# Kernel optimization log

Hardware: AMD Instinct MI355X
Metric: run time of the kernel (lower is better)

The kernel has to match this reference:

```python
import jax, jax.numpy as jnp
import numpy as np

# dims
B, T, E = 2, 4096, 512
H = 8
DH = E // H            # 64 per-head dim
DEPTH = 4
NHASH = 4              # n_hashes
BUCKET = 64            # bucket_size
NB = T // BUCKET       # n_buckets = 64 (even)
VOCAB, NCLASS = 32000, 10
FF = 4 * E
MASK_VAL = -1e9        # causal mask value
SELF_VAL = -5e4        # TOKEN_SELF_ATTN_VALUE


def layer_norm(x, g, b):
    m = jnp.mean(x, axis=-1, keepdims=True)
    v = jnp.var(x, axis=-1, keepdims=True)
    return (x - m) * jax.lax.rsqrt(v + 1e-5) * g + b


def lsh_attention(x, wqk, wv, wo, bo, rot):
    """Reformer LSH causal self-attention (eval mode, shared QK, n_hashes rounds)."""
    qk = (x @ wqk).reshape(B, T, H, DH).transpose(0, 2, 1, 3).reshape(B * H, T, DH)
    v = (x @ wv).reshape(B, T, H, DH).transpose(0, 2, 1, 3).reshape(B * H, T, DH)
    b = B * H
    # --- hash: random rotations -> bucket ids per hash round ---
    rotated = jnp.einsum('btf,fhi->bhti', qk, rot)             # (b, NHASH, T, NB//2)
    rotated = jnp.concatenate([rotated, -rotated], axis=-1)    # (b, NHASH, T, NB)
    buckets = jnp.argmax(rotated, axis=-1)                     # (b, NHASH, T)
    buckets = buckets + (jnp.arange(NHASH) * NB)[None, :, None]
    buckets = buckets.reshape(b, NHASH * T)
    # --- stable sort by (bucket, time) ---
    ticker = jnp.arange(NHASH * T)
    bt = buckets * T + (ticker % T)
    sticker = jnp.argsort(bt, axis=-1)                         # sort permutation
    undo_sort = jnp.argsort(sticker, axis=-1)
    st = sticker % T                                           # original time index of sorted slot
    sqk = jnp.take_along_axis(qk, st[..., None], axis=1)
    sv = jnp.take_along_axis(v, st[..., None], axis=1)
    # --- chunk into buckets, attend to own + previous chunk ---
    C = NHASH * NB                                             # number of chunks
    bq_t = st.reshape(b, C, BUCKET)
    bqk = sqk.reshape(b, C, BUCKET, DH)
    bv = sv.reshape(b, C, BUCKET, DH)
    bq = bqk
    bk = bqk / jnp.maximum(jnp.linalg.norm(bqk, axis=-1, keepdims=True), 1e-12)
    look = lambda t: jnp.concatenate([t, jnp.roll(t, 1, axis=1)], axis=2)
    bk, bvl, bkv_t = look(bk), look(bv), look(bq_t)
    dots = jnp.einsum('bcie,bcje->bcij', bq, bk) * (DH ** -0.5)  # (b, C, BUCKET, 2*BUCKET)
    causal = bq_t[:, :, :, None] < bkv_t[:, :, None, :]
    dots = jnp.where(causal, MASK_VAL, dots)
    self_m = bq_t[:, :, :, None] == bkv_t[:, :, None, :]
    dots = jnp.where(self_m, SELF_VAL, dots)
    lse = jax.nn.logsumexp(dots, axis=-1, keepdims=True)
    probs = jnp.exp(dots - lse)
    so = jnp.einsum('bcij,bcje->bcie', probs, bvl).reshape(b, NHASH * T, DH)
    slogits = lse.reshape(b, NHASH * T)
    # --- unsort and combine hash rounds via logsumexp weights ---
    o = jnp.take_along_axis(so, undo_sort[..., None], axis=1).reshape(b, NHASH, T, DH)
    logits = jnp.take_along_axis(slogits, undo_sort, axis=1).reshape(b, NHASH, T, 1)
    w = jnp.exp(logits - jax.nn.logsumexp(logits, axis=1, keepdims=True))
    out = jnp.sum(o * w, axis=1)                               # (b, T, DH)
    out = out.reshape(B, H, T, DH).transpose(0, 2, 1, 3).reshape(B, T, E)
    return out @ wo + bo


def feed_forward(x, w1, b1, w2, b2):
    return jax.nn.gelu(x @ w1 + b1, approximate=False) @ w2 + b2


def setup_inputs() -> dict:
    key = jax.random.key(0)
    ks = jax.random.split(key, 12)
    n = lambda k, s: (0.02 * jax.random.normal(k, s)).astype(jnp.float32)
    return {
        'x': jax.random.randint(ks[0], (B, T), 0, VOCAB),
        'tok_emb': n(ks[1], (VOCAB, E)),
        'pos_emb': n(ks[2], (T, E)),
        'rotations': jax.random.normal(ks[3], (DEPTH, DH, NHASH, NB // 2), dtype=jnp.float32),
        'ln1_g': jnp.ones((DEPTH, E), jnp.float32), 'ln1_b': jnp.zeros((DEPTH, E), jnp.float32),
        'w_qk': n(ks[4], (DEPTH, E, E)), 'w_v': n(ks[5], (DEPTH, E, E)),
        'w_o': n(ks[6], (DEPTH, E, E)), 'b_o': jnp.zeros((DEPTH, E), jnp.float32),
        'ln2_g': jnp.ones((DEPTH, E), jnp.float32), 'ln2_b': jnp.zeros((DEPTH, E), jnp.float32),
        'w_ff1': n(ks[7], (DEPTH, E, FF)), 'b_ff1': jnp.zeros((DEPTH, FF), jnp.float32),
        'w_ff2': n(ks[8], (DEPTH, FF, E)), 'b_ff2': jnp.zeros((DEPTH, E), jnp.float32),
        'w_final': n(ks[9], (E, NCLASS)), 'b_final': jnp.zeros((NCLASS,), jnp.float32),
    }


def reference(x, tok_emb, pos_emb, rotations, ln1_g, ln1_b, w_qk, w_v, w_o, b_o,
              ln2_g, ln2_b, w_ff1, b_ff1, w_ff2, b_ff2, w_final, b_final):
    h = tok_emb[x] + pos_emb[None, :, :]
    # reversible sequence: y1 = x1 + attn(ln(x2)); y2 = x2 + ff(ln(y1))
    x1, x2 = h, h
    for d in range(DEPTH):
        x1 = x1 + lsh_attention(layer_norm(x2, ln1_g[d], ln1_b[d]),
                                w_qk[d], w_v[d], w_o[d], b_o[d], rotations[d])
        x2 = x2 + feed_forward(layer_norm(x1, ln2_g[d], ln2_b[d]),
                               w_ff1[d], b_ff1[d], w_ff2[d], b_ff2[d])
    h = 0.5 * (x1 + x2)
    pooled = jnp.mean(h, axis=1)          # pooling == 'avg'
    return pooled @ w_final + b_final
```

## Files before the change

### kernel.cpp

```cpp
#include <hip/hip_runtime.h>
#include <hip/hip_bf16.h>
#include <math.h>

#define B_      2
#define T_      4096
#define E_      512
#define H_      8
#define DH_     64
#define DEPTH_  4
#define NHASH_  4
#define BUCKET_ 64
#define NB_     64
#define NB2_    32
#define C_      (NHASH_*NB_)
#define BH_     (B_*H_)
#define NT_     (NHASH_*T_)
#define FF_     2048
#define NCLASS_ 10
#define MASKV   (-1e9f)
#define SELFV   (-5e4f)

typedef __attribute__((ext_vector_type(8))) short short8;
typedef __attribute__((ext_vector_type(4))) float f32x4;

__device__ __forceinline__ void gload_lds16(const void* g, void* l) {
    __builtin_amdgcn_global_load_lds(
        (const __attribute__((address_space(1))) void*)g,
        (__attribute__((address_space(3))) void*)l,
        16, 0, 0);
}

__device__ __forceinline__ unsigned pk2(float a, float b) {
    __hip_bfloat16 ha = __float2bfloat16(a), hb = __float2bfloat16(b);
    unsigned short ua = *(unsigned short*)&ha, ub = *(unsigned short*)&hb;
    return (unsigned)ua | ((unsigned)ub << 16);
}

__global__ __launch_bounds__(128) void k_embed(const int* __restrict__ x, const float* __restrict__ tok,
                                               const float* __restrict__ pos, float* __restrict__ x1,
                                               float* __restrict__ x2)
{
    int bt = blockIdx.x;
    int t  = bt & (T_ - 1);
    int id = x[bt];
    float4 tv = ((const float4*)(tok + (size_t)id * E_))[threadIdx.x];
    float4 pv = ((const float4*)(pos + (size_t)t * E_))[threadIdx.x];
    float4 hv = make_float4(tv.x + pv.x, tv.y + pv.y, tv.z + pv.z, tv.w + pv.w);
    ((float4*)(x1 + (size_t)bt * E_))[threadIdx.x] = hv;
    ((float4*)(x2 + (size_t)bt * E_))[threadIdx.x] = hv;
}

template<bool LO>
__global__ __launch_bounds__(128) void k_ln(const float* __restrict__ in, const float* __restrict__ g,
                                            const float* __restrict__ b, __hip_bfloat16* __restrict__ out,
                                            __hip_bfloat16* __restrict__ outlo)
{
    int row = blockIdx.x, tid = threadIdx.x;
    float4 v = ((const float4*)(in + (size_t)row * E_))[tid];
    float s = v.x + v.y + v.z + v.w;
    float q = v.x * v.x + v.y * v.y + v.z * v.z + v.w * v.w;
#pragma unroll
    for (int d = 1; d < 64; d <<= 1) { s += __shfl_xor(s, d); q += __shfl_xor(q, d); }
    __shared__ float red[4];
    int w = tid >> 6;
    if ((tid & 63) == 0) { red[w * 2] = s; red[w * 2 + 1] = q; }
    __syncthreads();
    s = red[0] + red[2]; q = red[1] + red[3];
    float mean = s * (1.0f / E_);
    float var  = q * (1.0f / E_) - mean * mean;
    float rstd = rsqrtf(var + 1e-5f);
    float4 gv = ((const float4*)g)[tid];
    float4 bv = ((const float4*)b)[tid];
    float o0 = (v.x - mean) * rstd * gv.x + bv.x;
    float o1 = (v.y - mean) * rstd * gv.y + bv.y;
    float o2 = (v.z - mean) * rstd * gv.z + bv.z;
    float o3 = (v.w - mean) * rstd * gv.w + bv.w;
    __hip_bfloat16* op = out + (size_t)row * E_ + tid * 4;
    __hip_bfloat16 h0 = __float2bfloat16(o0), h1 = __float2bfloat16(o1);
    __hip_bfloat16 h2 = __float2bfloat16(o2), h3 = __float2bfloat16(o3);
    op[0] = h0; op[1] = h1; op[2] = h2; op[3] = h3;
    if (LO) {
        __hip_bfloat16* lp = outlo + (size_t)row * E_ + tid * 4;
        lp[0] = __float2bfloat16(o0 - __bfloat162float(h0));
        lp[1] = __float2bfloat16(o1 - __bfloat162float(h1));
        lp[2] = __float2bfloat16(o2 - __bfloat162float(h2));
        lp[3] = __float2bfloat16(o3 - __bfloat162float(h3));
    }
}

template<bool SPLIT>
__global__ __launch_bounds__(256) void k_wprep(const float* __restrict__ W, __hip_bfloat16* __restrict__ WT,
                                               __hip_bfloat16* __restrict__ WTlo, int K, int N)
{
    __shared__ float tile[32][33];
    int n0 = blockIdx.x * 32, k0 = blockIdx.y * 32;
    int tx = threadIdx.x & 31, ty = threadIdx.x >> 5;
#pragma unroll
    for (int i = 0; i < 4; ++i) {
        int k = ty + i * 8;
        tile[k][tx] = W[(size_t)(k0 + k) * N + n0 + tx];
    }
    __syncthreads();
#pragma unroll
    for (int i = 0; i < 4; ++i) {
        int n = ty + i * 8;
        float v = tile[tx][n];
        __hip_bfloat16 hv = __float2bfloat16(v);
        WT[(size_t)(n0 + n) * K + k0 + tx] = hv;
        if (SPLIT)
            WTlo[(size_t)(n0 + n) * K + k0 + tx] = __float2bfloat16(v - __bfloat162float(hv));
    }
}

__global__ __launch_bounds__(256) void k_rotprep(const float* __restrict__ rot,
                                                 __hip_bfloat16* __restrict__ rhs,
                                                 __hip_bfloat16* __restrict__ rls)
{
    int tid = threadIdx.x;
    for (int idx = tid; idx < 128 * 64; idx += 256) {
        int row = idx >> 6, f = idx & 63;
        float v = rot[(size_t)f * 128 + row];
        __hip_bfloat16 hv = __float2bfloat16(v);
        __hip_bfloat16 lv = __float2bfloat16(v - __bfloat162float(hv));
        int b = f >> 3;
        int off = row * 64 + (((b ^ (row & 7)) << 3) | (f & 7));
        rhs[off] = hv;
        rls[off] = lv;
    }
}

__device__ __forceinline__ float geluf(float xx) {
    return 0.5f * xx * (1.0f + erff(xx * 0.70710678118654752f));
}

template<int OUTK, int BIAS, int TM>
__global__ __launch_bounds__(256) void k_mgemm(const __hip_bfloat16* __restrict__ A,
                                               const __hip_bfloat16* __restrict__ WT,
                                               const float* __restrict__ bias, void* __restrict__ Cout,
                                               int N, int K, int nbnShift)
{
    constexpr int MF = TM / 32;
    constexpr int ABUF = TM * 64;
    __shared__ __align__(16) char smem[32768];
    char* AbBase = smem;
    char* BbBase = smem + 2 * ABUF;

    int tid = threadIdx.x;
    int lane = tid & 63, w = tid >> 6;
    int nwg = gridDim.x;
    int bid = blockIdx.x;
    int swz = (bid & 7) * (nwg >> 3) + (bid >> 3);
    int nmask = (1 << nbnShift) - 1;
    int m0 = (swz >> nbnShift) * TM, n0 = (swz & nmask) * 128;
    int wm = (w >> 1) * (TM / 2), wn = (w & 1) * 64;

    int r0 = tid >> 2, s0 = tid & 3;
    int c0 = (s0 - (r0 >> 1)) & 3;
    int r1 = r0 + 64;
    int c1 = (s0 - (r1 >> 1)) & 3;
    const __hip_bfloat16* aS0 = A  + (size_t)(m0 + r0) * K + c0 * 8;
    const __hip_bfloat16* aS1 = A  + (size_t)(m0 + r1) * K + c1 * 8;
    const __hip_bfloat16* bS0 = WT + (size_t)(n0 + r0) * K + c0 * 8;
    const __hip_bfloat16* bS1 = WT + (size_t)(n0 + r1) * K + c1 * 8;

    int cch = lane >> 4;
    int aoff[MF], boff[4];
#pragma unroll
    for (int f = 0; f < MF; ++f) {
        int ar = wm + f * 16 + (lane & 15);
        aoff[f] = ar * 32 + (((cch + (ar >> 1)) & 3) * 8);
    }
#pragma unroll
    for (int f = 0; f < 4; ++f) {
        int br = wn + f * 16 + (lane & 15);
        boff[f] = br * 32 + (((cch + (br >> 1)) & 3) * 8);
    }

    f32x4 acc[MF][4];
#pragma unroll
    for (int i = 0; i < MF; ++i)
#pragma unroll
        for (int j = 0; j < 4; ++j) acc[i][j] = (f32x4){0.f, 0.f, 0.f, 0.f};

    const int NS = K >> 5;
    {
        gload_lds16(aS0, AbBase + tid * 16);
        if constexpr (TM == 128) gload_lds16(aS1, AbBase + 4096 + tid * 16);
        gload_lds16(bS0, BbBase + tid * 16);
        gload_lds16(bS1, BbBase + 4096 + tid * 16);
    }
    __syncthreads();
    for (int s = 0; s < NS; ++s) {
        int cur = s & 1;
        if (s + 1 < NS) {
            int nb = cur ^ 1;
            int kk = (s + 1) * 32;
            char* Abn = AbBase + nb * ABUF;
            char* Bbn = BbBase + nb * 8192;
            gload_lds16(aS0 + kk, Abn + tid * 16);
            if constexpr (TM == 128) gload_lds16(aS1 + kk, Abn + 4096 + tid * 16);
            gload_lds16(bS0 + kk, Bbn + tid * 16);
            gload_lds16(bS1 + kk, Bbn + 4096 + tid * 16);
        }
        const __hip_bfloat16* Ab = (const __hip_bfloat16*)(AbBase + cur * ABUF);
        const __hip_bfloat16* Bb = (const __hip_bfloat16*)(BbBase + cur * 8192);
        short8 af[MF], bfr[4];
#pragma unroll
        for (int f = 0; f < MF; ++f) af[f] = *(const short8*)(Ab + aoff[f]);
#pragma unroll
        for (int f = 0; f < 4; ++f)  bfr[f] = *(const short8*)(Bb + boff[f]);
#pragma unroll
        for (int i = 0; i < MF; ++i)
#pragma unroll
            for (int j = 0; j < 4; ++j)
                acc[i][j] = __builtin_amdgcn_mfma_f32_16x16x32_bf16(af[i], bfr[j], acc[i][j], 0, 0, 0);
        __syncthreads();
    }

    int g = lane >> 4;
    if (OUTK == 2 || OUTK == 3) {
        unsigned short* Ot = (unsigned short*)smem;
#pragma unroll
        for (int i = 0; i < MF; ++i) {
#pragma unroll
            for (int j = 0; j < 4; ++j) {
                int col = wn + j * 16 + (lane & 15);
                float bv = BIAS ? bias[n0 + col] : 0.f;
#pragma unroll
                for (int q = 0; q < 4; ++q) {
                    int row = wm + i * 16 + g * 4 + q;
                    float vv = acc[i][j][q] + bv;
                    if (OUTK == 2) vv = geluf(vv);
                    __hip_bfloat16 hv = __float2bfloat16(vv);
                    Ot[row * 128 + (((col >> 3) ^ (row & 7)) << 3) + (col & 7)] = *(unsigned short*)&hv;
                }
            }
        }
        __syncthreads();
#pragma unroll
        for (int u = 0; u < TM / 16; ++u) {
            int f = u * 256 + tid;
            int row = f >> 4, cblk = f & 15;
            uint4 v = *(const uint4*)(Ot + row * 128 + ((cblk ^ (row & 7)) << 3));
            if (OUTK == 2) {
                *(uint4*)((__hip_bfloat16*)Cout + (size_t)(m0 + row) * N + n0 + cblk * 8) = v;
            } else {
                int mrow = m0 + row;
                int t = mrow & (T_ - 1), bI = mrow >> 12;
                int col = n0 + cblk * 8;
                int h = col >> 6, fin = col & 63;
                *(uint4*)((__hip_bfloat16*)Cout + ((size_t)(bI * H_ + h) * T_ + t) * 64 + fin) = v;
            }
        }
    } else if (TM == 64) {
        float* Ot = (float*)smem;
        float* Cb = (float*)Cout;
#pragma unroll
        for (int i = 0; i < MF; ++i) {
#pragma unroll
            for (int j = 0; j < 4; ++j) {
                int col = wn + j * 16 + (lane & 15);
#pragma unroll
                for (int q = 0; q < 4; ++q) {
                    int row = wm + i * 16 + g * 4 + q;
                    Ot[row * 128 + (((col >> 2) ^ (row & 7)) << 2) + (col & 3)] = acc[i][j][q];
                }
            }
        }
        __syncthreads();
#pragma unroll
        for (int u = 0; u < 8; ++u) {
            int f = u * 256 + tid;
            int row = f >> 5, c4 = f & 31;
            float4 v = *(const float4*)(Ot + row * 128 + ((c4 ^ (row & 7)) << 2));
            if (BIAS) {
                float4 bv = *(const float4*)(bias + n0 + c4 * 4);
                v.x += bv.x; v.y += bv.y; v.z += bv.z; v.w += bv.w;
            }
            float* cp = Cb + (size_t)(m0 + row) * N + n0 + c4 * 4;
            float4 old = *(const float4*)cp;
            v.x += old.x; v.y += old.y; v.z += old.z; v.w += old.w;
            *(float4*)cp = v;
        }
    } else {
        float* Ot = (float*)smem;
        float* Cb = (float*)Cout;
#pragma unroll
        for (int half = 0; half < 2; ++half) {
            if ((w >> 1) == half) {
#pragma unroll
                for (int i = 0; i < MF; ++i) {
#pragma unroll
                    for (int j = 0; j < 4; ++j) {
                        int col = wn + j * 16 + (lane & 15);
#pragma unroll
                        for (int q = 0; q < 4; ++q) {
                            int rowl = i * 16 + g * 4 + q;
                            Ot[rowl * 128 + (((col >> 2) ^ (rowl & 7)) << 2) + (col & 3)] = acc[i][j][q];
                        }
                    }
                }
            }
            __syncthreads();
#pragma unroll
            for (int u = 0; u < 8; ++u) {
                int f = u * 256 + tid;
                int row = f >> 5, c4 = f & 31;
                float4 v = *(const float4*)(Ot + row * 128 + ((c4 ^ (row & 7)) << 2));
                if (BIAS) {
                    float4 bv = *(const float4*)(bias + n0 + c4 * 4);
                    v.x += bv.x; v.y += bv.y; v.z += bv.z; v.w += bv.w;
                }
                float* cp = Cb + (size_t)(m0 + half * 64 + row) * N + n0 + c4 * 4;
                float4 old = *(const float4*)cp;
                v.x += old.x; v.y += old.y; v.z += old.z; v.w += old.w;
                *(float4*)cp = v;
            }
            __syncthreads();
        }
    }
}

#define STG_A(buf, kt, h) \
    gload_lds16(aSrc + (size_t)((h) * 128) * K + (kt) * 64,      smem + (buf) * 32768 + (h) * 16384 + tid * 16); \
    gload_lds16(aSrc + (size_t)((h) * 128 + 64) * K + (kt) * 64, smem + (buf) * 32768 + (h) * 16384 + 8192 + tid * 16);
#define STG_B(buf, kt, h) \
    gload_lds16(bSrc + (size_t)((h) * 128) * K + (kt) * 64,      smem + 65536 + (buf) * 32768 + (h) * 16384 + tid * 16); \
    gload_lds16(bSrc + (size_t)((h) * 128 + 64) * K + (kt) * 64, smem + 65536 + (buf) * 32768 + (h) * 16384 + 8192 + tid * 16);

#define PHASE8(buf, MH, NH, RA, RB, STAGE, GATE) do {                                             \
    const char* Ab_ = smem + (buf) * 32768;                                                       \
    const char* Bb_ = smem + 65536 + (buf) * 32768;                                               \
    STAGE                                                                                         \
    if (RA) {                                                                                     \
        _Pragma("unroll")                                                                         \
        for (int mf = 0; mf < 4; ++mf) {                                                          \
            int row = arow + (MH) * 128 + mf * 16;                                                \
            aF[mf][0] = *(const short8*)(Ab_ + row * 128 + sw0);                                  \
            aF[mf][1] = *(const short8*)(Ab_ + row * 128 + sw1);                                  \
        }                                                                                         \
    }                                                                                             \
    if (RB) {                                                                                     \
        _Pragma("unroll")                                                                         \
        for (int nf = 0; nf < 2; ++nf) {                                                          \
            int row = brow + (NH) * 128 + nf * 16;                                                \
            bF[nf][0] = *(const short8*)(Bb_ + row * 128 + sw0);                                  \
            bF[nf][1] = *(const short8*)(Bb_ + row * 128 + sw1);                                  \
        }                                                                                         \
    }                                                                                             \
    GATE                                                                                          \
    __builtin_amdgcn_s_barrier();                                                                 \
    asm volatile("s_waitcnt lgkmcnt(0)" ::: "memory");                                            \
    __builtin_amdgcn_sched_barrier(0);                                                            \
    __builtin_amdgcn_s_setprio(1);                                                                \
    _Pragma("unroll")                                                                             \
    for (int mf = 0; mf < 4; ++mf)                                                                \
        _Pragma("unroll")                                                                         \
        for (int nf = 0; nf < 2; ++nf) {                                                          \
            acc[MH][NH][mf][nf] = __builtin_amdgcn_mfma_f32_16x16x32_bf16(aF[mf][0], bF[nf][0], acc[MH][NH][mf][nf], 0, 0, 0); \
            acc[MH][NH][mf][nf] = __builtin_amdgcn_mfma_f32_16x16x32_bf16(aF[mf][1], bF[nf][1], acc[MH][NH][mf][nf], 0, 0, 0); \
        }                                                                                         \
    __builtin_amdgcn_s_setprio(0);                                                                \
    __builtin_amdgcn_s_barrier();                                                                 \
} while (0)

__global__ __launch_bounds__(512, 2) void k_gemm256_gelu(const __hip_bfloat16* __restrict__ A,
                                                         const __hip_bfloat16* __restrict__ WT,
                                                         const float* __restrict__ bias,
                                                         __hip_bfloat16* __restrict__ Cout,
                                                         int N, int K, int nShift)
{
    __shared__ __align__(16) char smem[131072];
    const int NT = K >> 6;
    int tid = threadIdx.x;
    int lane = tid & 63, w = tid >> 6;
    int lane7 = lane & 7, cch = lane >> 4;
    int nwg = gridDim.x;
    int bid = blockIdx.x;
    int swz = (bid & 7) * (nwg >> 3) + (bid >> 3);
    int m0 = (swz >> nShift) * 256;
    int n0 = (swz & ((1 << nShift) - 1)) * 256;

    int rstg = tid >> 3;
    int kcstg = (tid & 7) ^ (rstg & 7);
    const __hip_bfloat16* aSrc = A  + (size_t)(m0 + rstg) * K + kcstg * 8;
    const __hip_bfloat16* bSrc = WT + (size_t)(n0 + rstg) * K + kcstg * 8;

    int arow = (w >> 2) * 64 + (lane & 15);
    int brow = (w & 3) * 32 + (lane & 15);
    int sw0 = (cch ^ lane7) << 4;
    int sw1 = ((4 + cch) ^ lane7) << 4;

    f32x4 acc[2][2][4][2];
#pragma unroll
    for (int a2 = 0; a2 < 2; ++a2)
#pragma unroll
        for (int b2 = 0; b2 < 2; ++b2)
#pragma unroll
            for (int c2 = 0; c2 < 4; ++c2)
#pragma unroll
                for (int d2 = 0; d2 < 2; ++d2) acc[a2][b2][c2][d2] = (f32x4){0.f, 0.f, 0.f, 0.f};

    short8 aF[4][2], bF[2][2];

    STG_A(0, 0, 0) STG_A(0, 0, 1) STG_B(0, 0, 0) STG_B(0, 0, 1)
    if (NT > 1) { STG_A(1, 1, 0) STG_B(1, 1, 1) }
    if (NT > 1) asm volatile("s_waitcnt vmcnt(4)" ::: "memory");
    else        asm volatile("s_waitcnt vmcnt(0)" ::: "memory");
    __builtin_amdgcn_s_barrier();

    for (int t = 0; t < NT; ++t) {
        int buf = t & 1;
        PHASE8(buf, 0, 0, 1, 1, { if (t + 1 < NT) { STG_A(buf ^ 1, t + 1, 1) } }, {});
        PHASE8(buf, 0, 1, 0, 1, { if (t + 1 < NT) { STG_B(buf ^ 1, t + 1, 0) } }, {});
        PHASE8(buf, 1, 1, 1, 0, { if (t + 2 < NT) { STG_A(buf, t + 2, 0) } }, {});
        PHASE8(buf, 1, 0, 0, 1, { if (t + 2 < NT) { STG_B(buf, t + 2, 1) } },
               { if (t + 2 < NT)      asm volatile("s_waitcnt vmcnt(4)" ::: "memory");
                 else if (t + 1 < NT) asm volatile("s_waitcnt vmcnt(0)" ::: "memory"); });
    }

    unsigned short* Ot = (unsigned short*)smem;
    int g = lane >> 4;
#pragma unroll
    for (int mh = 0; mh < 2; ++mh)
#pragma unroll
        for (int nh = 0; nh < 2; ++nh)
#pragma unroll
            for (int nf = 0; nf < 2; ++nf) {
                int coll = nh * 128 + (w & 3) * 32 + nf * 16 + (lane & 15);
                float bv = bias[n0 + coll];
#pragma unroll
                for (int mf = 0; mf < 4; ++mf)
#pragma unroll
                    for (int q = 0; q < 4; ++q) {
                        int rowl = mh * 128 + (w >> 2) * 64 + mf * 16 + g * 4 + q;
                        float vv = geluf(acc[mh][nh][mf][nf][q] + bv);
                        __hip_bfloat16 hv = __float2bfloat16(vv);
                        Ot[rowl * 256 + ((((coll >> 4) ^ (rowl & 7)) << 4) | (coll & 15))] = *(unsigned short*)&hv;
                    }
            }
    __syncthreads();
#pragma unroll
    for (int u = 0; u < 16; ++u) {
        int f = u * 512 + tid;
        int rowl = f >> 5, c16 = f & 31;
        uint4 v = *(const uint4*)(Ot + rowl * 256 + ((((c16 >> 1) ^ (rowl & 7)) << 4) | ((c16 & 1) << 3)));
        *(uint4*)(Cout + (size_t)(m0 + rowl) * N + n0 + c16 * 8) = v;
    }
}
#undef PHASE8
#undef STG_A
#undef STG_B

__global__ __launch_bounds__(256) void k_mgemm_qk(const __hip_bfloat16* __restrict__ Ah,
                                                  const __hip_bfloat16* __restrict__ Al,
                                                  const __hip_bfloat16* __restrict__ Bh,
                                                  const __hip_bfloat16* __restrict__ Bl,
                                                  float* __restrict__ Cout)
{
    __shared__ __align__(16) char smem[49152];
    const int N = 512, K = 512;
    int tid = threadIdx.x;
    int lane = tid & 63, w = tid >> 6;
    int nwg = gridDim.x;
    int bid = blockIdx.x;
    int swz = (bid & 7) * (nwg >> 3) + (bid >> 3);
    int m0 = (swz >> 2) * 64, n0 = (swz & 3) * 128;
    int wm = (w >> 1) * 32, wn = (w & 1) * 64;

    int r0 = tid >> 2, s0 = tid & 3;
    int c0 = (s0 - (r0 >> 1)) & 3;
    int r1 = r0 + 64;
    int c1 = (s0 - (r1 >> 1)) & 3;
    const __hip_bfloat16* ahS  = Ah + (size_t)(m0 + r0) * K + c0 * 8;
    const __hip_bfloat16* alS  = Al + (size_t)(m0 + r0) * K + c0 * 8;
    const __hip_bfloat16* bhS0 = Bh + (size_t)(n0 + r0) * K + c0 * 8;
    const __hip_bfloat16* bhS1 = Bh + (size_t)(n0 + r1) * K + c1 * 8;
    const __hip_bfloat16* blS0 = Bl + (size_t)(n0 + r0) * K + c0 * 8;
    const __hip_bfloat16* blS1 = Bl + (size_t)(n0 + r1) * K + c1 * 8;

    int cch = lane >> 4;
    int aoff[2], boff[4];
#pragma unroll
    for (int f = 0; f < 2; ++f) {
        int ar = wm + f * 16 + (lane & 15);
        aoff[f] = ar * 32 + (((cch + (ar >> 1)) & 3) * 8);
    }
#pragma unroll
    for (int f = 0; f < 4; ++f) {
        int br = wn + f * 16 + (lane & 15);
        boff[f] = br * 32 + (((cch + (br >> 1)) & 3) * 8);
    }

    f32x4 acc[2][4];
#pragma unroll
    for (int i = 0; i < 2; ++i)
#pragma unroll
        for (int j = 0; j < 4; ++j) acc[i][j] = (f32x4){0.f, 0.f, 0.f, 0.f};

#define QK_STAGE(buf, kk)                                                     \
    { char* bb = smem + (buf) * 24576;                                        \
      gload_lds16(ahS  + (kk), bb + tid * 16);                                \
      gload_lds16(alS  + (kk), bb + 4096  + tid * 16);                        \
      gload_lds16(bhS0 + (kk), bb + 8192  + tid * 16);                        \
      gload_lds16(bhS1 + (kk), bb + 12288 + tid * 16);                        \
      gload_lds16(blS0 + (kk), bb + 16384 + tid * 16);                        \
      gload_lds16(blS1 + (kk), bb + 20480 + tid * 16); }

    QK_STAGE(0, 0)
    __syncthreads();
    const int NS = K >> 5;
    for (int s = 0; s < NS; ++s) {
        int cur = s & 1;
        if (s + 1 < NS) QK_STAGE(cur ^ 1, (s + 1) * 32)
        const __hip_bfloat16* AhB = (const __hip_bfloat16*)(smem + cur * 24576);
        const __hip_bfloat16* AlB = (const __hip_bfloat16*)(smem + cur * 24576 + 4096);
        const __hip_bfloat16* BhB = (const __hip_bfloat16*)(smem + cur * 24576 + 8192);
        const __hip_bfloat16* BlB = (const __hip_bfloat16*)(smem + cur * 24576 + 16384);
        short8 afh[2], afl[2], bfh[4], bfl[4];
#pragma unroll
        for (int f = 0; f < 2; ++f) {
            afh[f] = *(const short8*)(AhB + aoff[f]);
            afl[f] = *(const short8*)(AlB + aoff[f]);
        }
#pragma unroll
        for (int f = 0; f < 4; ++f) {
            bfh[f] = *(const short8*)(BhB + boff[f]);
            bfl[f] = *(const short8*)(BlB + boff[f]);
        }
#pragma unroll
        for (int i = 0; i < 2; ++i)
#pragma unroll
            for (int j = 0; j < 4; ++j) {
                acc[i][j] = __builtin_amdgcn_mfma_f32_16x16x32_bf16(afh[i], bfh[j], acc[i][j], 0, 0, 0);
                acc[i][j] = __builtin_amdgcn_mfma_f32_16x16x32_bf16(afh[i], bfl[j], acc[i][j], 0, 0, 0);
                acc[i][j] = __builtin_amdgcn_mfma_f32_16x16x32_bf16(afl[i], bfh[j], acc[i][j], 0, 0, 0);
            }
        __syncthreads();
    }
#undef QK_STAGE

    int g = lane >> 4;
    float* Ot = (float*)smem;
#pragma unroll
    for (int i = 0; i < 2; ++i) {
#pragma unroll
        for (int j = 0; j < 4; ++j) {
            int col = wn + j * 16 + (lane & 15);
#pragma unroll
            for (int q = 0; q < 4; ++q) {
                int row = wm + i * 16 + g * 4 + q;
                Ot[row * 128 + (((col >> 2) ^ (row & 7)) << 2) + (col & 3)] = acc[i][j][q];
            }
        }
    }
    __syncthreads();
#pragma unroll
    for (int u = 0; u < 8; ++u) {
        int f = u * 256 + tid;
        int row = f >> 5, c4 = f & 31;
        float4 v = *(const float4*)(Ot + row * 128 + ((c4 ^ (row & 7)) << 2));
        *(float4*)(Cout + (size_t)(m0 + row) * N + n0 + c4 * 4) = v;
    }
}

__global__ __launch_bounds__(256) void k_hash(const float* __restrict__ qk,
                                              const __hip_bfloat16* __restrict__ rhs,
                                              const __hip_bfloat16* __restrict__ rls,
                                              unsigned char* __restrict__ bkt,
                                              __hip_bfloat16* __restrict__ qh,
                                              __hip_bfloat16* __restrict__ kh)
{
    __shared__ __align__(16) char smem[65536];
    char* RH = smem;
    char* RL = smem + 16384;
    char* QH = smem + 32768;
    char* QL = smem + 49152;
    int tid = threadIdx.x, lane = tid & 63, wv = tid >> 6;
    int bh = blockIdx.x, tc = blockIdx.y;
    int bI = bh >> 3, h = bh & 7;

#pragma unroll
    for (int it = 0; it < 4; ++it) {
        gload_lds16((const char*)rhs + it * 4096 + tid * 16, RH + it * 4096 + tid * 16);
        gload_lds16((const char*)rls + it * 4096 + tid * 16, RL + it * 4096 + tid * 16);
    }

    {
        int t = tid >> 1, half = tid & 1;
        int tg = tc * 128 + t;
        const float4* qsrc = (const float4*)(qk + ((size_t)(bI * T_ + tg)) * E_ + h * DH_ + half * 32);
        float4 q4[8];
        float n2 = 0.f;
#pragma unroll
        for (int j = 0; j < 8; ++j) {
            q4[j] = qsrc[j];
            n2 += q4[j].x * q4[j].x + q4[j].y * q4[j].y + q4[j].z * q4[j].z + q4[j].w * q4[j].w;
        }
        n2 += __shfl_xor(n2, 1);
        float sc = 0.125f / fmaxf(sqrtf(n2), 1e-12f);
        float qv[32];
#pragma unroll
        for (int j = 0; j < 8; ++j) {
            qv[4 * j] = q4[j].x; qv[4 * j + 1] = q4[j].y; qv[4 * j + 2] = q4[j].z; qv[4 * j + 3] = q4[j].w;
        }
        unsigned short hb[32], lb[32], kb[32];
#pragma unroll
        for (int j = 0; j < 32; ++j) {
            __hip_bfloat16 hv = __float2bfloat16(qv[j]);
            __hip_bfloat16 lv = __float2bfloat16(qv[j] - __bfloat162float(hv));
            __hip_bfloat16 kv = __float2bfloat16(qv[j] * sc);
            hb[j] = *(unsigned short*)&hv; lb[j] = *(unsigned short*)&lv; kb[j] = *(unsigned short*)&kv;
        }
        size_t ro = ((size_t)bh * T_ + tg) * 64 + half * 32;
        uint4* qdst = (uint4*)(qh + ro);
        uint4* kdst = (uint4*)(kh + ro);
#pragma unroll
        for (int j = 0; j < 4; ++j) {
            qdst[j] = *(uint4*)&hb[8 * j];
            kdst[j] = *(uint4*)&kb[8 * j];
        }
#pragma unroll
        for (int j = 0; j < 4; ++j) {
            int b = half * 4 + j;
            int xo = t * 128 + ((b ^ (t & 7)) << 4);
            *(uint4*)(QH + xo) = *(uint4*)&hb[8 * j];
            *(uint4*)(QL + xo) = *(uint4*)&lb[8 * j];
        }
    }
    __syncthreads();

#pragma unroll
    for (int sub = 0; sub < 2; ++sub) {
        int tl = wv * 32 + sub * 16 + (lane & 15);
        int g = lane >> 4;
        short8 qfh0 = *(const short8*)(QH + tl * 128 + ((g ^ (tl & 7)) << 4));
        short8 qfh1 = *(const short8*)(QH + tl * 128 + (((4 + g) ^ (tl & 7)) << 4));
        short8 qfl0 = *(const short8*)(QL + tl * 128 + ((g ^ (tl & 7)) << 4));
        short8 qfl1 = *(const short8*)(QL + tl * 128 + (((4 + g) ^ (tl & 7)) << 4));
        f32x4 sacc[8];
#pragma unroll
        for (int kt = 0; kt < 8; ++kt) sacc[kt] = (f32x4){0.f, 0.f, 0.f, 0.f};
#pragma unroll
        for (int kt = 0; kt < 8; ++kt) {
            int row = kt * 16 + (lane & 15);
            short8 rh0 = *(const short8*)(RH + row * 128 + ((g ^ (row & 7)) << 4));
            short8 rh1 = *(const short8*)(RH + row * 128 + (((4 + g) ^ (row & 7)) << 4));
            short8 rl0 = *(const short8*)(RL + row * 128 + ((g ^ (row & 7)) << 4));
            short8 rl1 = *(const short8*)(RL + row * 128 + (((4 + g) ^ (row & 7)) << 4));
            sacc[kt] = __builtin_amdgcn_mfma_f32_16x16x32_bf16(rh0, qfh0, sacc[kt], 0, 0, 0);
            sacc[kt] = __builtin_amdgcn_mfma_f32_16x16x32_bf16(rh1, qfh1, sacc[kt], 0, 0, 0);
            sacc[kt] = __builtin_amdgcn_mfma_f32_16x16x32_bf16(rl0, qfh0, sacc[kt], 0, 0, 0);
            sacc[kt] = __builtin_amdgcn_mfma_f32_16x16x32_bf16(rl1, qfh1, sacc[kt], 0, 0, 0);
            sacc[kt] = __builtin_amdgcn_mfma_f32_16x16x32_bf16(rh0, qfl0, sacc[kt], 0, 0, 0);
            sacc[kt] = __builtin_amdgcn_mfma_f32_16x16x32_bf16(rh1, qfl1, sacc[kt], 0, 0, 0);
        }
#pragma unroll
        for (int rd = 0; rd < 4; ++rd) {
            float bv = -3.0e38f; int bi = 0;
#pragma unroll
            for (int kp = 0; kp < 2; ++kp) {
#pragma unroll
                for (int rr = 0; rr < 4; ++rr) {
                    int i = kp * 16 + g * 4 + rr;
                    float v = sacc[rd * 2 + kp][rr];
                    if (v > bv) { bv = v; bi = i; }
                }
            }
#pragma unroll
            for (int kp = 0; kp < 2; ++kp) {
#pragma unroll
                for (int rr = 0; rr < 4; ++rr) {
                    int i = 32 + kp * 16 + g * 4 + rr;
                    float v = -sacc[rd * 2 + kp][rr];
                    if (v > bv) { bv = v; bi = i; }
                }
            }
#pragma unroll
            for (int dlt = 16; dlt <= 32; dlt <<= 1) {
                float ov = __shfl_xor(bv, dlt);
                int oi = __shfl_xor(bi, dlt);
                if (ov > bv || (ov == bv && oi < bi)) { bv = ov; bi = oi; }
            }
            if (g == 0)
                bkt[((size_t)(bh * NHASH_ + rd)) * T_ + tc * 128 + tl] = (unsigned char)bi;
        }
    }
}

__global__ __launch_bounds__(64) void k_sort(const unsigned char* __restrict__ bkt, int* __restrict__ st)
{
    __shared__ unsigned char bktL[T_];
    __shared__ int hist[64][65];
    __shared__ int goff[NB_];
    int tid = threadIdx.x;
    int bhr = blockIdx.x;
    const unsigned char* src = bkt + (size_t)bhr * T_;
#pragma unroll
    for (int i = 0; i < 4; ++i)
        ((uint4*)bktL)[tid * 4 + i] = ((const uint4*)src)[tid * 4 + i];
#pragma unroll
    for (int j = 0; j < 16; ++j) ((int4*)&hist[tid][0])[j] = make_int4(0, 0, 0, 0);
    int base = tid * 64;
#pragma unroll 8
    for (int i = 0; i < 64; ++i) hist[tid][bktL[base + i]]++;
    __syncthreads();
    int run = 0;
#pragma unroll 8
    for (int s = 0; s < 64; ++s) { int v = hist[s][tid]; hist[s][tid] = run; run += v; }
    int tot = run;
    int pre = tot;
#pragma unroll
    for (int d = 1; d < 64; d <<= 1) { int o = __shfl_up(pre, d); if (tid >= d) pre += o; }
    goff[tid] = pre - tot;
    __syncthreads();
#pragma unroll 8
    for (int b = 0; b < 64; ++b) hist[tid][b] += goff[b];
    int* dst = st + (size_t)bhr * T_;
#pragma unroll 8
    for (int i = 0; i < 64; ++i) {
        int b = bktL[base + i];
        int off = hist[tid][b]++;
        dst[off] = base + i;
    }
}

__global__ __launch_bounds__(256, 2) void k_attn(const __hip_bfloat16* __restrict__ qh,
                                                 const __hip_bfloat16* __restrict__ kh,
                                                 const __hip_bfloat16* __restrict__ vh,
                                                 const int* __restrict__ st,
                                                 __hip_bfloat16* __restrict__ o,
                                                 float* __restrict__ lg)
{
    __shared__ __align__(16) char smem[49664];
    char* KbB = smem;
    char* VtB = smem + 16384;
    char* PbB = smem + 32768;
    int*  kvt = (int*)(smem + 49152);
    unsigned short* ObU = (unsigned short*)smem;

    int tid = threadIdx.x;
    int lane = tid & 63;
    int g = lane >> 4;
    int wv = tid >> 6;
    int wq0 = wv * 16;

    int bid = blockIdx.x;
    int bh = ((bid & 7) << 1) | ((bid >> 3) & 1);
    int c  = bid >> 4;
    int rnd = c >> 6;
    int cp = (c + C_ - 1) & (C_ - 1);
    const size_t stB = (size_t)bh * NT_;

    if (tid < 128) {
        int cc = (tid < 64) ? c : cp;
        kvt[tid] = st[stB + (size_t)cc * 64 + (tid & 63)];
    }
    __syncthreads();

    {
        int k = tid >> 1, half = tid & 1;
        const uint4* src = (const uint4*)(kh + ((size_t)bh * T_ + kvt[k]) * 64 + half * 32);
#pragma unroll
        for (int j2 = 0; j2 < 4; ++j2) {
            uint4 a = src[j2];
            int blk = (half * 4 + j2) ^ (k & 7);
            *(uint4*)(KbB + k * 128 + blk * 16) = a;
        }
    }
    {
        int kp = tid & 63, dq = tid >> 6;
        const uint4* r0 = (const uint4*)(vh + ((size_t)bh * T_ + kvt[2 * kp]) * 64 + dq * 16);
        const uint4* r1 = (const uint4*)(vh + ((size_t)bh * T_ + kvt[2 * kp + 1]) * 64 + dq * 16);
        unsigned short va[16], vb2[16];
        *(uint4*)&va[0] = r0[0];  *(uint4*)&va[8] = r0[1];
        *(uint4*)&vb2[0] = r1[0]; *(uint4*)&vb2[8] = r1[1];
#pragma unroll
        for (int i = 0; i < 16; ++i) {
            int d = dq * 16 + i;
            unsigned wrd = (unsigned)va[i] | ((unsigned)vb2[i] << 16);
            *(unsigned*)(VtB + d * 256 + ((((kp >> 2) ^ i)) << 4) + ((kp & 3) << 2)) = wrd;
        }
    }
    int tq = kvt[wq0 + (lane & 15)];
    const __hip_bfloat16* qrow = qh + ((size_t)bh * T_ + tq) * 64;
    short8 qf0 = *(const short8*)(qrow + g * 8);
    short8 qf1 = *(const short8*)(qrow + 32 + g * 8);
    __syncthreads();

    f32x4 sacc[8];
#pragma unroll
    for (int kt = 0; kt < 8; ++kt) sacc[kt] = (f32x4){0.f, 0.f, 0.f, 0.f};
#pragma unroll
    for (int kt = 0; kt < 8; ++kt) {
        int row = kt * 16 + (lane & 15);
        short8 kf0 = *(const short8*)(KbB + row * 128 + (((g) ^ (row & 7)) << 4));
        short8 kf1 = *(const short8*)(KbB + row * 128 + (((4 + g) ^ (row & 7)) << 4));
        sacc[kt] = __builtin_amdgcn_mfma_f32_16x16x32_bf16(kf0, qf0, sacc[kt], 0, 0, 0);
        sacc[kt] = __builtin_amdgcn_mfma_f32_16x16x32_bf16(kf1, qf1, sacc[kt], 0, 0, 0);
    }

    float m = -3.0e38f;
#pragma unroll
    for (int kt = 0; kt < 8; ++kt) {
#pragma unroll
        for (int r = 0; r < 4; ++r) {
            int tk = kvt[kt * 16 + g * 4 + r];
            float dd = sacc[kt][r];
            dd = (tk > tq) ? MASKV : dd;
            dd = (tk == tq) ? SELFV : dd;
            sacc[kt][r] = dd;
            m = fmaxf(m, dd);
        }
    }
    m = fmaxf(m, __shfl_xor(m, 16));
    m = fmaxf(m, __shfl_xor(m, 32));
    float ssum = 0.f;
#pragma unroll
    for (int kt = 0; kt < 8; ++kt) {
        float p0 = __expf(sacc[kt][0] - m);
        float p1 = __expf(sacc[kt][1] - m);
        float p2 = __expf(sacc[kt][2] - m);
        float p3 = __expf(sacc[kt][3] - m);
        ssum += (p0 + p1) + (p2 + p3);
        uint2 wrd = make_uint2(pk2(p0, p1), pk2(p2, p3));
        int blk = (kt * 2 + (g >> 1)) ^ (lane & 15);
        *(uint2*)(PbB + (wq0 + (lane & 15)) * 256 + (blk << 4) + ((g & 1) << 3)) = wrd;
    }
    ssum += __shfl_xor(ssum, 16);
    ssum += __shfl_xor(ssum, 32);
    if (lane < 16)
        lg[stB + (size_t)rnd * T_ + tq] = m + __logf(ssum);

    f32x4 pacc[4];
#pragma unroll
    for (int dt = 0; dt < 4; ++dt) pacc[dt] = (f32x4){0.f, 0.f, 0.f, 0.f};
#pragma unroll
    for (int s = 0; s < 4; ++s) {
        int xr = ((s * 4 + g) ^ (lane & 15)) << 4;
        short8 pf = *(const short8*)(PbB + (wq0 + (lane & 15)) * 256 + xr);
#pragma unroll
        for (int dt = 0; dt < 4; ++dt) {
            short8 vf = *(const short8*)(VtB + (dt * 16 + (lane & 15)) * 256 + xr);
            pacc[dt] = __builtin_amdgcn_mfma_f32_16x16x32_bf16(pf, vf, pacc[dt], 0, 0, 0);
        }
    }
    __syncthreads();

#pragma unroll
    for (int r = 0; r < 4; ++r) {
        float sr = __shfl(ssum, g * 4 + r);
        float inv = 1.0f / sr;
        int rowl = wq0 + g * 4 + r;
#pragma unroll
        for (int dt = 0; dt < 4; ++dt) {
            __hip_bfloat16 hv = __float2bfloat16(pacc[dt][r] * inv);
            ObU[rowl * 72 + dt * 16 + (lane & 15)] = *(unsigned short*)&hv;
        }
    }
    __syncthreads();

    {
        int rr = tid >> 2, seg = tid & 3;
        uint4 a = *(const uint4*)(ObU + rr * 72 + seg * 16);
        uint4 b = *(const uint4*)(ObU + rr * 72 + seg * 16 + 8);
        size_t jor = stB + (size_t)rnd * T_ + kvt[rr];
        uint4* dst = (uint4*)(o + jor * 64 + seg * 16);
        dst[0] = a; dst[1] = b;
    }
}

__global__ __launch_bounds__(256) void k_combine(const __hip_bfloat16* __restrict__ o,
                                                 const float* __restrict__ lg,
                                                 __hip_bfloat16* __restrict__ att)
{
    int bt = blockIdx.x;
    int bI = bt >> 12;
    int t  = bt & (T_ - 1);
    for (int e = threadIdx.x; e < E_; e += 256) {
        int h = e >> 6, f = e & 63;
        size_t base = ((size_t)(bI * H_ + h)) * NT_ + t;
        float L0 = lg[base], L1 = lg[base + T_], L2 = lg[base + 2 * T_], L3 = lg[base + 3 * T_];
        float M = fmaxf(fmaxf(L0, L1), fmaxf(L2, L3));
        float w0 = __expf(L0 - M), w1 = __expf(L1 - M), w2 = __expf(L2 - M), w3 = __expf(L3 - M);
        float sw = w0 + w1 + w2 + w3;
        float val = __bfloat162float(o[base * DH_ + f]) * w0
                  + __bfloat162float(o[(base + T_) * DH_ + f]) * w1
                  + __bfloat162float(o[(base + 2 * T_) * DH_ + f]) * w2
                  + __bfloat162float(o[(base + 3 * T_) * DH_ + f]) * w3;
        att[(size_t)bt * E_ + e] = __float2bfloat16(val / sw);
    }
}

__global__ __launch_bounds__(256) void k_pool1(const float* __restrict__ x1, const float* __restrict__ x2,
                                               float* __restrict__ part)
{
    int blk = blockIdx.x;
    int bI = blk >> 5, tc = blk & 31;
    int t0 = tc * 128;
    for (int e = threadIdx.x; e < E_; e += 256) {
        float s = 0.f;
        for (int t = t0; t < t0 + 128; ++t) {
            size_t idx = ((size_t)bI * T_ + t) * E_ + e;
            s += x1[idx] + x2[idx];
        }
        part[((size_t)bI * 32 + tc) * E_ + e] = s;
    }
}

__global__ __launch_bounds__(256) void k_final(const float* __restrict__ part, const float* __restrict__ wf,
                                               const float* __restrict__ bf, float* __restrict__ out)
{
    __shared__ float pooled[B_ * E_];
    int tid = threadIdx.x;
    for (int i = tid; i < B_ * E_; i += 256) {
        int bI = i >> 9, e = i & 511;
        float s = 0.f;
        for (int c2 = 0; c2 < 32; ++c2) s += part[((size_t)bI * 32 + c2) * E_ + e];
        pooled[i] = s * (0.5f / T_);
    }
    __syncthreads();
    if (tid < B_ * NCLASS_) {
        int bI = tid / NCLASS_, cl = tid % NCLASS_;
        float s = bf[cl];
        for (int e = 0; e < E_; ++e) s += pooled[bI * E_ + e] * wf[(size_t)e * NCLASS_ + cl];
        out[tid] = s;
    }
}

extern "C" void kernel_launch(void* const* d_in, const int* in_sizes, int n_in,
                              void* d_out, int out_size, void* d_ws, size_t ws_size,
                              hipStream_t stream)
{
    const int*   X    = (const int*)d_in[0];
    const float* TOK  = (const float*)d_in[1];
    const float* POS  = (const float*)d_in[2];
    const float* ROT  = (const float*)d_in[3];
    const float* LN1G = (const float*)d_in[4];
    const float* LN1B = (const float*)d_in[5];
    const float* WQK  = (const float*)d_in[6];
    const float* WV   = (const float*)d_in[7];
    const float* WO   = (const float*)d_in[8];
    const float* BO   = (const float*)d_in[9];
    const float* LN2G = (const float*)d_in[10];
    const float* LN2B = (const float*)d_in[11];
    const float* WF1  = (const float*)d_in[12];
    const float* BF1  = (const float*)d_in[13];
    const float* WF2  = (const float*)d_in[14];
    const float* BF2  = (const float*)d_in[15];
    const float* WFIN = (const float*)d_in[16];
    const float* BFIN = (const float*)d_in[17];

    float* ws = (float*)d_ws;
    const size_t S = (size_t)B_ * T_ * E_;
    float* x1   = ws;
    float* x2   = x1 + S;
    float* qkb  = x2 + S;
    float* vb   = qkb + S;
    float* bigf = vb + S;
    float* lgb  = bigf + 2 * S;
    float* part = lgb + (size_t)BH_ * NT_;
    __hip_bfloat16* lnbh  = (__hip_bfloat16*)(part + (size_t)B_ * 32 * E_);
    __hip_bfloat16* lnbl  = lnbh + S;
    __hip_bfloat16* attnb = lnbl + S;
    int*   stb  = (int*)(attnb + S);
    __hip_bfloat16* WTbase = (__hip_bfloat16*)(stb + (size_t)BH_ * NT_);
    __hip_bfloat16* big    = (__hip_bfloat16*)bigf;

    const size_t W55 = (size_t)512 * 512;
    const size_t WFF = (size_t)2048 * 512;
    __hip_bfloat16* WTqk_hi = WTbase;
    __hip_bfloat16* WTqk_lo = WTqk_hi + 4 * W55;
    __hip_bfloat16* WTv     = WTqk_lo + 4 * W55;
    __hip_bfloat16* WTo     = WTv     + 4 * W55;
    __hip_bfloat16* WTf1    = WTo     + 4 * W55;
    __hip_bfloat16* WTf2    = WTf1    + 4 * WFF;
    unsigned char*  bktb    = (unsigned char*)(WTf2 + 4 * WFF);
    __hip_bfloat16* qh      = (__hip_bfloat16*)(bktb + (size_t)BH_ * NHASH_ * T_);
    __hip_bfloat16* khb     = qh  + (size_t)BH_ * T_ * 64;
    __hip_bfloat16* vhb     = khb + (size_t)BH_ * T_ * 64;
    __hip_bfloat16* rswzh   = vhb + (size_t)BH_ * T_ * 64;
    __hip_bfloat16* rswzl   = rswzh + 4 * 8192;

    for (int d = 0; d < DEPTH_; ++d) {
        k_wprep<true ><<<dim3(16, 16), 256, 0, stream>>>(WQK + d * W55, WTqk_hi + d * W55,
                                                         WTqk_lo + d * W55, 512, 512);
        k_wprep<false><<<dim3(16, 16), 256, 0, stream>>>(WV + d * W55, WTv + d * W55, nullptr, 512, 512);
        k_wprep<false><<<dim3(16, 16), 256, 0, stream>>>(WO + d * W55, WTo + d * W55, nullptr, 512, 512);
        k_wprep<false><<<dim3(64, 16), 256, 0, stream>>>(WF1 + d * WFF, WTf1 + d * WFF, nullptr, 512, 2048);
        k_wprep<false><<<dim3(16, 64), 256, 0, stream>>>(WF2 + d * WFF, WTf2 + d * WFF, nullptr, 2048, 512);
        k_rotprep<<<1, 256, 0, stream>>>(ROT + (size_t)d * 64 * 128, rswzh + d * 8192, rswzl + d * 8192);
    }

    const int g512_64 = (512 / 128) * ((B_ * T_) / 64);
    const int gff1    = ((B_ * T_) / 256) * (FF_ / 256);

    k_embed<<<B_ * T_, 128, 0, stream>>>(X, TOK, POS, x1, x2);
    for (int d = 0; d < DEPTH_; ++d) {
        k_ln<true><<<B_ * T_, 128, 0, stream>>>(x2, LN1G + (size_t)d * E_, LN1B + (size_t)d * E_, lnbh, lnbl);
        k_mgemm_qk<<<g512_64, 256, 0, stream>>>(lnbh, lnbl, WTqk_hi + d * W55, WTqk_lo + d * W55, qkb);
        k_mgemm<3, 0, 64><<<g512_64, 256, 0, stream>>>(lnbh, WTv + d * W55, nullptr, vhb, 512, 512, 2);
        k_hash<<<dim3(BH_, T_ / 128), 256, 0, stream>>>(qkb, rswzh + d * 8192, rswzl + d * 8192,
                                                        bktb, qh, khb);
        k_sort<<<BH_ * NHASH_, 64, 0, stream>>>(bktb, stb);
        k_attn<<<BH_ * C_, 256, 0, stream>>>(qh, khb, vhb, stb, big, lgb);
        k_combine<<<B_ * T_, 256, 0, stream>>>(big, lgb, attnb);
        k_mgemm<1, 1, 64><<<g512_64, 256, 0, stream>>>(attnb, WTo + d * W55, BO + (size_t)d * E_, x1,
                                                       512, 512, 2);
        k_ln<false><<<B_ * T_, 128, 0, stream>>>(x1, LN2G + (size_t)d * E_, LN2B + (size_t)d * E_, lnbh, nullptr);
        k_gemm256_gelu<<<gff1, 512, 0, stream>>>(lnbh, WTf1 + d * WFF, BF1 + (size_t)d * FF_, big,
                                                 2048, 512, 3);
        k_mgemm<1, 1, 64><<<g512_64, 256, 0, stream>>>(big, WTf2 + d * WFF, BF2 + (size_t)d * E_, x2,
                                                       512, 2048, 2);
    }
    k_pool1<<<B_ * 32, 256, 0, stream>>>(x1, x2, part);
    k_final<<<1, 256, 0, stream>>>(part, WFIN, BFIN, (float*)d_out);
}
```

Measured before the change: 878.7 us.

## Interleave hash-round outputs per token, precompute combine weights, approximate GELU erf

Result: faster. 858.7 us (-2.3%).

```diff
diff --git a/kernel.cpp b/kernel.cpp
--- a/kernel.cpp
+++ b/kernel.cpp
@@ -129,8 +129,15 @@
     }
 }
 
-__device__ __forceinline__ float geluf(float xx) {
-    return 0.5f * xx * (1.0f + erff(xx * 0.70710678118654752f));
+__device__ __forceinline__ float geluf(float x) {
+    float ax = fabsf(x) * 0.70710678118654752f;
+    float t  = __builtin_amdgcn_rcpf(1.0f + 0.3275911f * ax);
+    float poly = t * (0.254829592f + t * (-0.284496736f + t * (1.421413741f +
+                 t * (-1.453152027f + t * 1.061405429f))));
+    float e = __expf(-ax * ax);
+    float erfax = 1.0f - poly * e;
+    float erfx = copysignf(erfax, x);
+    return 0.5f * x * (1.0f + erfx);
 }
 
 template<int OUTK, int BIAS, int TM>
@@ -830,7 +837,7 @@
     ssum += __shfl_xor(ssum, 16);
     ssum += __shfl_xor(ssum, 32);
     if (lane < 16)
-        lg[stB + (size_t)rnd * T_ + tq] = m + __logf(ssum);
+        lg[((size_t)bh * T_ + tq) * 4 + rnd] = m + __logf(ssum);
 
     f32x4 pacc[4];
 #pragma unroll
@@ -864,8 +871,8 @@
         int rr = tid >> 2, seg = tid & 3;
         uint4 a = *(const uint4*)(ObU + rr * 72 + seg * 16);
         uint4 b = *(const uint4*)(ObU + rr * 72 + seg * 16 + 8);
-        size_t jor = stB + (size_t)rnd * T_ + kvt[rr];
-        uint4* dst = (uint4*)(o + jor * 64 + seg * 16);
+        size_t jor = (size_t)bh * T_ + kvt[rr];
+        uint4* dst = (uint4*)(o + jor * 256 + rnd * 64 + seg * 16);
         dst[0] = a; dst[1] = b;
     }
 }
@@ -874,21 +881,30 @@
                                                  const float* __restrict__ lg,
                                                  __hip_bfloat16* __restrict__ att)
 {
+    __shared__ float ws[H_][8];
     int bt = blockIdx.x;
     int bI = bt >> 12;
     int t  = bt & (T_ - 1);
-    for (int e = threadIdx.x; e < E_; e += 256) {
+    int tid = threadIdx.x;
+    if (tid < H_) {
+        size_t base = ((size_t)(bI * H_ + tid) * T_ + t);
+        float4 L = *(const float4*)(lg + base * 4);
+        float M = fmaxf(fmaxf(L.x, L.y), fmaxf(L.z, L.w));
+        float w0 = __expf(L.x - M), w1 = __expf(L.y - M), w2 = __expf(L.z - M), w3 = __expf(L.w - M);
+        float inv = 1.0f / (w0 + w1 + w2 + w3);
+        ws[tid][0] = w0 * inv; ws[tid][1] = w1 * inv; ws[tid][2] = w2 * inv; ws[tid][3] = w3 * inv;
+    }
+    __syncthreads();
+#pragma unroll
+    for (int it = 0; it < 2; ++it) {
+        int e = it * 256 + tid;
         int h = e >> 6, f = e & 63;
-        size_t base = ((size_t)(bI * H_ + h)) * NT_ + t;
-        float L0 = lg[base], L1 = lg[base + T_], L2 = lg[base + 2 * T_], L3 = lg[base + 3 * T_];
-        float M = fmaxf(fmaxf(L0, L1), fmaxf(L2, L3));
-        float w0 = __expf(L0 - M), w1 = __expf(L1 - M), w2 = __expf(L2 - M), w3 = __expf(L3 - M);
-        float sw = w0 + w1 + w2 + w3;
-        float val = __bfloat162float(o[base * DH_ + f]) * w0
-                  + __bfloat162float(o[(base + T_) * DH_ + f]) * w1
-                  + __bfloat162float(o[(base + 2 * T_) * DH_ + f]) * w2
-                  + __bfloat162float(o[(base + 3 * T_) * DH_ + f]) * w3;
-        att[(size_t)bt * E_ + e] = __float2bfloat16(val / sw);
+        const __hip_bfloat16* op = o + ((size_t)(bI * H_ + h) * T_ + t) * 256;
+        float val = __bfloat162float(op[f])       * ws[h][0]
+                  + __bfloat162float(op[64 + f])  * ws[h][1]
+                  + __bfloat162float(op[128 + f]) * ws[h][2]
+                  + __bfloat162float(op[192 + f]) * ws[h][3];
+        att[(size_t)bt * E_ + e] = __float2bfloat16(val);
     }
 }
 
```
